# Optimization experiments

Hardware: AMD Instinct MI355X
Metric: run time of the kernel (lower is better)

Reference implementation:

```python
import jax, jax.numpy as jnp
import numpy as np

HEADS = 3
FILT = 16
V_FEATS = 11
N_NODES = 100000
E_INT = 400000
E_NH = 1600000
ATT_SIZE = FILT * 2 * HEADS            # 96
DENSE_IN = ATT_SIZE * HEADS            # 288


def setup_inputs() -> dict:
    key = jax.random.key(0)
    ks = jax.random.split(key, 12)
    node_feats = jax.random.normal(ks[0], (N_NODES, V_FEATS), dtype=jnp.float32)
    edge_int = jax.random.randint(ks[1], (2, E_INT), 0, N_NODES, dtype=jnp.int64)
    edge_nh = jax.random.randint(ks[2], (2, E_NH), 0, N_NODES, dtype=jnp.int64)
    s = 0.1
    W_int = jax.random.normal(ks[3], (V_FEATS, HEADS * FILT), dtype=jnp.float32) * s
    a_src_int = jax.random.normal(ks[4], (HEADS, FILT), dtype=jnp.float32) * s
    a_dst_int = jax.random.normal(ks[5], (HEADS, FILT), dtype=jnp.float32) * s
    W_nh = jax.random.normal(ks[6], (V_FEATS, HEADS * FILT), dtype=jnp.float32) * s
    a_src_nh = jax.random.normal(ks[7], (HEADS, FILT), dtype=jnp.float32) * s
    a_dst_nh = jax.random.normal(ks[8], (HEADS, FILT), dtype=jnp.float32) * s
    att_w = jax.random.normal(ks[9], (ATT_SIZE, HEADS), dtype=jnp.float32) * s
    dense_w = jax.random.normal(ks[10], (DENSE_IN, 1), dtype=jnp.float32) * s
    dense_b = jnp.zeros((1,), dtype=jnp.float32)
    return {
        "node_feats": node_feats,
        "W_int": W_int, "a_src_int": a_src_int, "a_dst_int": a_dst_int,
        "W_nh": W_nh, "a_src_nh": a_src_nh, "a_dst_nh": a_dst_nh,
        "att_w": att_w, "dense_w": dense_w, "dense_b": dense_b,
        "edge_int": edge_int, "edge_nh": edge_nh,
    }


def _gat(x, edges, W, a_src, a_dst):
    """Graph-attention branch: gather -> edge softmax (per dst) -> scatter-add."""
    n = x.shape[0]
    h = (x @ W).reshape(n, HEADS, FILT)              # [N,H,F]
    src, dst = edges[0], edges[1]
    e_s = jnp.einsum('nhf,hf->nh', h, a_src)         # [N,H]
    e_d = jnp.einsum('nhf,hf->nh', h, a_dst)
    e = jax.nn.leaky_relu(e_s[src] + e_d[dst], 0.2)  # [E,H]
    m = jax.ops.segment_max(e, dst, num_segments=n)  # per-dst max for stability
    m = jnp.where(jnp.isfinite(m), m, 0.0)
    p = jnp.exp(e - m[dst])
    denom = jax.ops.segment_sum(p, dst, num_segments=n)
    alpha = p / (denom[dst] + 1e-16)                 # [E,H]
    out = jax.ops.segment_sum(alpha[:, :, None] * h[src], dst, num_segments=n)
    return out.reshape(n, HEADS * FILT)              # [N,48]


def reference(node_feats, W_int, a_src_int, a_dst_int, W_nh, a_src_nh, a_dst_nh,
              att_w, dense_w, dense_b, edge_int, edge_nh):
    x_int = _gat(node_feats, edge_int, W_int, a_src_int, a_dst_int)   # [N,48]
    x_nh = _gat(node_feats, edge_nh, W_nh, a_src_nh, a_dst_nh)        # [N,48]
    x = jnp.concatenate((x_int, x_nh), axis=1)                        # [N,96]
    # multi-head self-attention pooling over nodes
    scores = jnp.tanh(x @ att_w)                                      # [N,3]
    alpha = jax.nn.softmax(scores, axis=0)                            # softmax over nodes
    rep = jnp.einsum('nh,nd->hd', alpha, x).reshape(-1)               # [288]
    out = rep @ dense_w + dense_b                                     # [1]
    return out
```

## Files before the change

kernel.cpp:

```cpp
#include <hip/hip_runtime.h>
#include <math.h>

#define HEADS 3
#define FILT 16
#define HF 48
#define VF 11

#define NBGP 2048
#define NBINMAX 512
#define CAP0 4096
#define CAP1 8192
#define SCCH 8192

typedef unsigned int uint;
typedef unsigned short ushort;

__device__ inline uint f2bf(float x) {
    uint u = __float_as_uint(x);
    return (u + 0x7FFFu + ((u >> 16) & 1u)) >> 16;
}

__device__ inline float tanh_fast(float s) {
    const float sc = fminf(fmaxf(s, -15.f), 15.f);
    const float t = __expf(2.f * sc);
    return (t - 1.f) / (t + 1.f);
}


__global__ __launch_bounds__(256) void k_nodes(
    const float* __restrict__ nf,
    const float* __restrict__ W_int, const float* __restrict__ as_int, const float* __restrict__ ad_int,
    const float* __restrict__ W_nh,  const float* __restrict__ as_nh,  const float* __restrict__ ad_nh,
    float* __restrict__ ws, int* __restrict__ binfill, int N)
{
    __shared__ float sW0[VF*HF], sW1[VF*HF];
    __shared__ float sa[4][HF];
    __shared__ float sF[64*VF];
    __shared__ uint  sH[64*32];
    const int t = threadIdx.x;
    for (int i = t; i < VF*HF; i += 256) { sW0[i] = W_int[i]; sW1[i] = W_nh[i]; }
    if (t < HF) { sa[0][t] = as_int[t]; sa[1][t] = ad_int[t]; sa[2][t] = as_nh[t]; sa[3][t] = ad_nh[t]; }

    const long Nl = N;
    const long B0 = (long)blockIdx.x * 64;
    {
        const long idx = (long)blockIdx.x * 256 + t;
        if (idx < 2*NBINMAX) binfill[idx] = 0;
    }
    for (int i = t; i < 64*VF; i += 256) {
        const long g = B0*VF + i;
        sF[i] = (g < Nl*VF) ? nf[g] : 0.f;
    }
    __syncthreads();

    const int nl = t >> 2;
    const int q  = t & 3;
    const long n = B0 + nl;
    const bool valid = n < Nl;

    float f[VF];
    #pragma unroll
    for (int v = 0; v < VF; v++) f[v] = sF[nl*VF + v];

    for (int b = 0; b < 2; b++) {
        if (b == 1) __syncthreads();
        const float* W = b ? sW1 : sW0;
        float acc[12];
        #pragma unroll
        for (int j = 0; j < 12; j++) acc[j] = 0.f;
        #pragma unroll
        for (int v = 0; v < VF; v++) {
            const float fv = f[v];
            #pragma unroll
            for (int j = 0; j < 12; j++)
                acc[j] = fmaf(fv, W[v*HF + q*12 + j], acc[j]);
        }
        #pragma unroll
        for (int i = 0; i < 6; i++)
            sH[nl*32 + q*6 + i] = f2bf(acc[2*i]) | (f2bf(acc[2*i+1]) << 16);
        sH[nl*32 + 24 + 2*q + 0] = 0u;
        sH[nl*32 + 24 + 2*q + 1] = 0u;

        float s0=0.f,s1=0.f,s2=0.f,d0=0.f,d1=0.f,d2=0.f;
        #pragma unroll
        for (int j = 0; j < 12; j++) {
            const int fg = q*12 + j;
            const int hd = fg >> 4;
            const float ps = acc[j] * sa[2*b + 0][fg];
            const float pd = acc[j] * sa[2*b + 1][fg];
            s0 += (hd == 0) ? ps : 0.f;  d0 += (hd == 0) ? pd : 0.f;
            s1 += (hd == 1) ? ps : 0.f;  d1 += (hd == 1) ? pd : 0.f;
            s2 += (hd == 2) ? ps : 0.f;  d2 += (hd == 2) ? pd : 0.f;
        }
        s0 += __shfl_xor(s0,1); s0 += __shfl_xor(s0,2);
        s1 += __shfl_xor(s1,1); s1 += __shfl_xor(s1,2);
        s2 += __shfl_xor(s2,1); s2 += __shfl_xor(s2,2);
        d0 += __shfl_xor(d0,1); d0 += __shfl_xor(d0,2);
        d1 += __shfl_xor(d1,1); d1 += __shfl_xor(d1,2);
        d2 += __shfl_xor(d2,1); d2 += __shfl_xor(d2,2);
        if (valid && q == 0) {
            float* ES = ws + 64*Nl + (b ? 8*Nl : 0);
            float* ED = ES + 4*Nl;
            ((float4*)ES)[n] = make_float4(s0, s1, s2, 0.f);
            ((float4*)ED)[n] = make_float4(d0, d1, d2, 0.f);
        }
        __syncthreads();
        uint* Hg = (uint*)(ws + (b ? 32*Nl : 0));
        for (int i = t; i < 64*32; i += 256) {
            const long node = B0 + (i >> 5);
            if (node < Nl) Hg[B0*32 + i] = sH[i];
        }
    }
}

__global__ __launch_bounds__(256) void k_binscatter(
    const int* __restrict__ e0, int E0, int nb0,
    const int* __restrict__ e1, int E1,
    int* __restrict__ binfill, uint* __restrict__ pk0, uint* __restrict__ pk1)
{
    __shared__ int lh[NBINMAX], lb[NBINMAX];
    const int b = blockIdx.x;
    const int* e; long E; int* bf; uint* pk; int bb, cap;
    if (b < nb0) { e = e0; E = E0; bf = binfill;           pk = pk0; bb = b;       cap = CAP0; }
    else         { e = e1; E = E1; bf = binfill + NBINMAX; pk = pk1; bb = b - nb0; cap = CAP1; }
    for (int i = threadIdx.x; i < NBINMAX; i += 256) lh[i] = 0;
    __syncthreads();
    const int t = threadIdx.x;
    const long base = (long)bb * SCCH;
    #pragma unroll 4
    for (int k = 0; k < SCCH/256; k++) {
        const long i = base + (long)k*256 + t;
        if (i < E) atomicAdd(&lh[e[E + i] >> 8], 1);
    }
    __syncthreads();
    for (int i = t; i < NBINMAX; i += 256) {
        const int c = lh[i];
        lb[i] = c ? atomicAdd(&bf[i], c) : 0;
        lh[i] = 0;
    }
    __syncthreads();
    #pragma unroll 4
    for (int k = 0; k < SCCH/256; k++) {
        const long i = base + (long)k*256 + t;
        if (i < E) {
            const int s = e[i];
            const int d = e[E + i];
            const int bin = d >> 8;
            const int off = atomicAdd(&lh[bin], 1);
            pk[(long)bin*cap + lb[bin] + off] = ((uint)(d & 255) << 17) | (uint)s;
        }
    }
}

__global__ __launch_bounds__(256) void k_binbucket(
    const uint* __restrict__ pk0, const uint* __restrict__ pk1,
    const int* __restrict__ binfill, int nbin,
    int2* __restrict__ ms0, int* __restrict__ bk0,
    int2* __restrict__ ms1, int* __restrict__ bk1, int N)
{
    __shared__ int nc[256], ns[256], wsum[4];
    const int b = blockIdx.x;
    const int br = (b < nbin) ? 0 : 1;
    const int bin = b - br*nbin;
    const uint* pk = br ? pk1 : pk0;
    const int cap  = br ? CAP1 : CAP0;
    int2* ms = br ? ms1 : ms0;
    int* bk  = br ? bk1 : bk0;
    const long pbase = (long)bin * cap;
    const int m = binfill[br*NBINMAX + bin];
    const int t = threadIdx.x, lane = t & 63, wid = t >> 6;

    nc[t] = 0;
    __syncthreads();
    for (int i = t; i < m; i += 256)
        atomicAdd(&nc[(pk[pbase + i] >> 17) & 255], 1);
    __syncthreads();
    const int v = nc[t];
    int x = v;
    #pragma unroll
    for (int d = 1; d < 64; d <<= 1) { const int u = __shfl_up(x, d); if (lane >= d) x += u; }
    if (lane == 63) wsum[wid] = x;
    __syncthreads();
    int wb = 0;
    #pragma unroll
    for (int w = 0; w < 4; w++) if (w < wid) wb += wsum[w];
    ns[t] = wb + x - v;
    const int n = bin*256 + t;
    if (n < N) ms[n] = make_int2(v, (int)pbase + ns[t] + v);
    nc[t] = 0;
    __syncthreads();
    for (int i = t; i < m; i += 256) {
        const uint p = pk[pbase + i];
        const int dl = (p >> 17) & 255;
        const int off = atomicAdd(&nc[dl], 1);
        bk[pbase + ns[dl] + off] = (int)(p & 0x1FFFFu);
    }
}

__global__ __launch_bounds__(256) void k_gp(
    const uint* __restrict__ H0, const uint* __restrict__ H1,
    const float* __restrict__ ES0, const float4* __restrict__ ED0,
    const float* __restrict__ ES1, const float4* __restrict__ ED1,
    const int2* __restrict__ ms0, const int* __restrict__ bk0,
    const int2* __restrict__ ms1, const int* __restrict__ bk1,
    const float* __restrict__ att_w, const float* __restrict__ dense_w,
    float* __restrict__ gpart, int N)
{
    __shared__ int   sIdx[4][4*64];
    __shared__ float sP[4][4*192];
    const int t = threadIdx.x, lane = t & 63, wid = t >> 6;
    const int half = lane >> 5;
    const int hl = lane & 31;
    const int hcc = (hl >> 3) < 3 ? (hl >> 3) : 2;

    float cL0[3]={0,0,0}, cH0[3]={0,0,0}, cL1[3]={0,0,0}, cH1[3]={0,0,0};
    if (hl < 24) {
        const int f0 = 2*hl, f1 = f0 + 1;
        #pragma unroll
        for (int k = 0; k < 3; k++) {
            if (half == 0) {
                cL0[k] = att_w[f0*3 + k];        cH0[k] = att_w[f1*3 + k];
                cL1[k] = att_w[(HF+f0)*3 + k];   cH1[k] = att_w[(HF+f1)*3 + k];
            } else {
                cL0[k] = dense_w[k*96 + f0];     cH0[k] = dense_w[k*96 + f1];
                cL1[k] = dense_w[k*96 + HF+f0];  cH1[k] = dense_w[k*96 + HF+f1];
            }
        }
    }

    int* iw = sIdx[wid];
    float* pw = sP[wid];

    float acc6[6] = {0,0,0,0,0,0};
    const int gw = blockIdx.x*4 + wid;
    const int nw = NBGP*4;

    for (int n = gw; n < N; n += 2*nw) {
        const int nB = n + nw;
        const bool hasB = nB < N;
        const int2 m0t = ms0[n];
        const int2 m1t = ms1[n];
        const int2 m2t = hasB ? ms0[nB] : make_int2(0, 0);
        const int2 m3t = hasB ? ms1[nB] : make_int2(0, 0);
        int deg[4] = {m0t.x, m1t.x, m2t.x, m3t.x};
        int bas[4] = {m0t.y - m0t.x, m1t.y - m1t.x, m2t.y - m2t.x, m3t.y - m3t.x};
        const int mx = max(max(deg[0], deg[1]), max(deg[2], deg[3]));

        float xL[4], xH[4];

        if (mx <= 64) {
            float4 ev[4];
            ev[0] = ED0[n]; ev[1] = ED1[n];
            ev[2] = hasB ? ED0[nB] : make_float4(0,0,0,0);
            ev[3] = hasB ? ED1[nB] : make_float4(0,0,0,0);
            int sv[4];
            sv[0] = (lane < deg[0]) ? bk0[bas[0] + lane] : 0;
            sv[1] = (lane < deg[1]) ? bk1[bas[1] + lane] : 0;
            sv[2] = (lane < deg[2]) ? bk0[bas[2] + lane] : 0;
            sv[3] = (lane < deg[3]) ? bk1[bas[3] + lane] : 0;
            float4 es[4];
            es[0] = ((const float4*)ES0)[sv[0]];
            es[1] = ((const float4*)ES1)[sv[1]];
            es[2] = ((const float4*)ES0)[sv[2]];
            es[3] = ((const float4*)ES1)[sv[3]];
            #pragma unroll
            for (int T = 0; T < 4; T++) {
                float v0 = es[T].x + ev[T].x, v1 = es[T].y + ev[T].y, v2 = es[T].z + ev[T].z;
                v0 = fmaxf(v0, 0.2f*v0);
                v1 = fmaxf(v1, 0.2f*v1);
                v2 = fmaxf(v2, 0.2f*v2);
                const bool a = lane < deg[T];
                const float p0 = a ? __expf(v0) : 0.f;
                const float p1 = a ? __expf(v1) : 0.f;
                const float p2 = a ? __expf(v2) : 0.f;
                iw[T*64 + lane] = sv[T];
                pw[T*192 + lane*3 + 0] = p0;
                pw[T*192 + lane*3 + 1] = p1;
                pw[T*192 + lane*3 + 2] = p2;
            }
            float accL[4] = {0,0,0,0}, accH[4] = {0,0,0,0}, den[4] = {0,0,0,0};
            const int R = (mx + 7) >> 3;
            for (int r = 0; r < R; r++) {
                const int j0 = r*8;
                uint w[4][4]; float q[4][4];
                #pragma unroll
                for (int T = 0; T < 4; T++) {
                    const uint* H = (T & 1) ? H1 : H0;
                    if (j0 < deg[T]) {
                        #pragma unroll
                        for (int u = 0; u < 4; u++) {
                            const int ei = j0 + 2*u + half;
                            q[T][u] = pw[T*192 + ei*3 + hcc];
                            w[T][u] = H[(long)iw[T*64 + ei]*32 + hl];
                        }
                    }
                }
                #pragma unroll
                for (int T = 0; T < 4; T++) {
                    if (j0 < deg[T]) {
                        #pragma unroll
                        for (int u = 0; u < 4; u++) {
                            accL[T] = fmaf(q[T][u], __uint_as_float(w[T][u] << 16), accL[T]);
                            accH[T] = fmaf(q[T][u], __uint_as_float(w[T][u] & 0xFFFF0000u), accH[T]);
                            den[T] += q[T][u];
                        }
                    }
                }
            }
            #pragma unroll
            for (int T = 0; T < 4; T++) {
                accL[T] += __shfl_xor(accL[T], 32);
                accH[T] += __shfl_xor(accH[T], 32);
                den[T]  += __shfl_xor(den[T], 32);
                const float dinv = 1.f / (den[T] + 1e-16f);
                xL[T] = accL[T] * dinv;
                xH[T] = accH[T] * dinv;
            }
        } else {
            #pragma unroll
            for (int T = 0; T < 4; T++) {
                const uint* H   = (T & 1) ? H1 : H0;
                const float* ES = (T & 1) ? ES1 : ES0;
                const float4* ED = (T & 1) ? ED1 : ED0;
                const int* bk   = (T & 1) ? bk1 : bk0;
                const int nn    = (T >> 1) ? nB : n;
                float accL = 0.f, accH = 0.f, dn = 0.f;
                if (deg[T] > 0) {
                    const float4 edv = ED[nn];
                    for (int e0 = 0; e0 < deg[T]; e0 += 64) {
                        int m = deg[T] - e0; if (m > 64) m = 64;
                        int srcv = 0; float p0 = 0.f, p1 = 0.f, p2 = 0.f;
                        if (lane < m) {
                            srcv = bk[bas[T] + e0 + lane];
                            const float4 esv = ((const float4*)ES)[srcv];
                            float v0 = esv.x + edv.x, v1 = esv.y + edv.y, v2 = esv.z + edv.z;
                            v0 = fmaxf(v0, 0.2f*v0);
                            v1 = fmaxf(v1, 0.2f*v1);
                            v2 = fmaxf(v2, 0.2f*v2);
                            p0 = __expf(v0); p1 = __expf(v1); p2 = __expf(v2);
                        }
                        iw[lane] = srcv;
                        pw[lane*3 + 0] = p0; pw[lane*3 + 1] = p1; pw[lane*3 + 2] = p2;
                        for (int j = 0; j < m; j += 2) {
                            const int ei = j + half;
                            const float qq = pw[ei*3 + hcc];
                            const uint wv = H[(long)iw[ei]*32 + hl];
                            accL = fmaf(qq, __uint_as_float(wv << 16), accL);
                            accH = fmaf(qq, __uint_as_float(wv & 0xFFFF0000u), accH);
                            dn += qq;
                        }
                    }
                }
                accL += __shfl_xor(accL, 32);
                accH += __shfl_xor(accH, 32);
                dn   += __shfl_xor(dn, 32);
                const float dinv = 1.f / (dn + 1e-16f);
                xL[T] = accL * dinv;
                xH[T] = accH * dinv;
            }
        }

        #pragma unroll
        for (int s = 0; s < 2; s++) {
            if (s == 1 && !hasB) break;
            float rr[3];
            #pragma unroll
            for (int k = 0; k < 3; k++)
                rr[k] = xL[2*s]*cL0[k] + xH[2*s]*cH0[k] + xL[2*s+1]*cL1[k] + xH[2*s+1]*cH1[k];
            #pragma unroll
            for (int k = 0; k < 3; k++) {
                #pragma unroll
                for (int o = 1; o < 32; o <<= 1) rr[k] += __shfl_xor(rr[k], o);
            }
            float oo[3];
            #pragma unroll
            for (int k = 0; k < 3; k++) oo[k] = __shfl_xor(rr[k], 32);
            if (lane == 0) {
                #pragma unroll
                for (int k = 0; k < 3; k++) {
                    const float e = __expf(tanh_fast(rr[k]));
                    acc6[k]   += e;
                    acc6[3+k] += e * oo[k];
                }
            }
        }
    }

    __shared__ float red[4][6];
    if (lane == 0) {
        #pragma unroll
        for (int k = 0; k < 6; k++) red[wid][k] = acc6[k];
    }
    __syncthreads();
    if (t < 6) gpart[(long)blockIdx.x*6 + t] = red[0][t] + red[1][t] + red[2][t] + red[3][t];
}

__global__ __launch_bounds__(1024) void k_final(const float* __restrict__ gpart, int nb,
                                                const float* __restrict__ dense_b,
                                                float* __restrict__ out)
{
    const int t = threadIdx.x, lane = t & 63, wid = t >> 6;
    float acc[6] = {0.f,0.f,0.f,0.f,0.f,0.f};
    for (long i = t; i < nb; i += 1024) {
        #pragma unroll
        for (int k = 0; k < 6; k++) acc[k] += gpart[i*6 + k];
    }
    __shared__ float red[16][6];
    #pragma unroll
    for (int k = 0; k < 6; k++) {
        float v = acc[k];
        #pragma unroll
        for (int o = 32; o > 0; o >>= 1) v += __shfl_xor(v, o);
        if (lane == 0) red[wid][k] = v;
    }
    __syncthreads();
    if (t == 0) {
        float tot[6] = {0.f,0.f,0.f,0.f,0.f,0.f};
        #pragma unroll
        for (int w = 0; w < 16; w++)
            #pragma unroll
            for (int k = 0; k < 6; k++) tot[k] += red[w][k];
        float o = dense_b[0];
        #pragma unroll
        for (int h = 0; h < HEADS; h++) o += tot[3 + h] / tot[h];
        out[0] = o;
    }
}

extern "C" void kernel_launch(void* const* d_in, const int* in_sizes, int n_in,
                              void* d_out, int out_size, void* d_ws, size_t ws_size,
                              hipStream_t stream)
{
    const float* nf      = (const float*)d_in[0];
    const float* W_int   = (const float*)d_in[1];
    const float* as_int  = (const float*)d_in[2];
    const float* ad_int  = (const float*)d_in[3];
    const float* W_nh    = (const float*)d_in[4];
    const float* as_nh   = (const float*)d_in[5];
    const float* ad_nh   = (const float*)d_in[6];
    const float* att_w   = (const float*)d_in[7];
    const float* dense_w = (const float*)d_in[8];
    const float* dense_b = (const float*)d_in[9];
    const int*   e_int   = (const int*)d_in[10];
    const int*   e_nh    = (const int*)d_in[11];

    const int N  = in_sizes[0] / VF;
    const int E0 = in_sizes[10] / 2;
    const int E1 = in_sizes[11] / 2;
    const int nbin = (N + 255) >> 8;

    float* ws = (float*)d_ws;
    const long Nl = N;

    uint* h0 = (uint*)ws;
    uint* h1 = (uint*)(ws + 32*Nl);
    float* es0 = ws + 64*Nl;
    float4* ed0 = (float4*)(ws + 68*Nl);
    float* es1 = ws + 72*Nl;
    float4* ed1 = (float4*)(ws + 76*Nl);
    int2* ms0 = (int2*)(ws + 80*Nl);
    int2* ms1 = (int2*)(ws + 82*Nl);
    int* binfill = (int*)(ws + 84*Nl);
    uint* pk0 = (uint*)(binfill + 2*NBINMAX);
    uint* pk1 = pk0 + (long)nbin*CAP0;
    int* bk0  = (int*)(pk1 + (long)nbin*CAP1);
    int* bk1  = bk0 + (long)nbin*CAP0;
    float* gpart = (float*)(bk1 + (long)nbin*CAP1);

    const int nbK1 = (N + 63) / 64;
    const int nbs0 = (E0 + SCCH - 1) / SCCH;
    const int nbs1 = (E1 + SCCH - 1) / SCCH;

    k_nodes<<<nbK1, 256, 0, stream>>>(nf, W_int, as_int, ad_int, W_nh, as_nh, ad_nh,
                                      ws, binfill, N);
    k_binscatter<<<nbs0 + nbs1, 256, 0, stream>>>(e_int, E0, nbs0, e_nh, E1,
                                                  binfill, pk0, pk1);
    k_binbucket<<<2*nbin, 256, 0, stream>>>(pk0, pk1, binfill, nbin,
                                            ms0, bk0, ms1, bk1, N);
    k_gp<<<NBGP, 256, 0, stream>>>(h0, h1, es0, ed0, es1, ed1,
                                   ms0, bk0, ms1, bk1,
                                   att_w, dense_w, gpart, N);
    k_final<<<1, 1024, 0, stream>>>(gpart, NBGP, dense_b, (float*)d_out);
}
```

Before: 146.4 us.

## Process GAT branches in separate passes with per-node partial projections stored

The gather kernel now runs the two graph branches in two sequential passes, handling four nodes of the same branch per wave iteration instead of two nodes across both branches. The first pass writes per-node partial attention scores and dense projections into a scratch buffer that reuses the packed-edge workspace. The second pass adds its own partials and accumulates the pooling sums. The aim is better locality, since each pass gathers from only one feature table, at the cost of an extra per-node write and read and a second sweep over the nodes.

Result: slower. 188.7 us (+28.9%).

```diff
diff --git a/kernel.cpp b/kernel.cpp
--- a/kernel.cpp
+++ b/kernel.cpp
@@ -204,7 +204,7 @@
     const int2* __restrict__ ms0, const int* __restrict__ bk0,
     const int2* __restrict__ ms1, const int* __restrict__ bk1,
     const float* __restrict__ att_w, const float* __restrict__ dense_w,
-    float* __restrict__ gpart, int N)
+    float* __restrict__ pd, float* __restrict__ gpart, int N)
 {
     __shared__ int   sIdx[4][4*64];
     __shared__ float sP[4][4*192];
@@ -235,152 +235,162 @@
     const int gw = blockIdx.x*4 + wid;
     const int nw = NBGP*4;
 
-    for (int n = gw; n < N; n += 2*nw) {
-        const int nB = n + nw;
-        const bool hasB = nB < N;
-        const int2 m0t = ms0[n];
-        const int2 m1t = ms1[n];
-        const int2 m2t = hasB ? ms0[nB] : make_int2(0, 0);
-        const int2 m3t = hasB ? ms1[nB] : make_int2(0, 0);
-        int deg[4] = {m0t.x, m1t.x, m2t.x, m3t.x};
-        int bas[4] = {m0t.y - m0t.x, m1t.y - m1t.x, m2t.y - m2t.x, m3t.y - m3t.x};
-        const int mx = max(max(deg[0], deg[1]), max(deg[2], deg[3]));
-
-        float xL[4], xH[4];
-
-        if (mx <= 64) {
-            float4 ev[4];
-            ev[0] = ED0[n]; ev[1] = ED1[n];
-            ev[2] = hasB ? ED0[nB] : make_float4(0,0,0,0);
-            ev[3] = hasB ? ED1[nB] : make_float4(0,0,0,0);
-            int sv[4];
-            sv[0] = (lane < deg[0]) ? bk0[bas[0] + lane] : 0;
-            sv[1] = (lane < deg[1]) ? bk1[bas[1] + lane] : 0;
-            sv[2] = (lane < deg[2]) ? bk0[bas[2] + lane] : 0;
-            sv[3] = (lane < deg[3]) ? bk1[bas[3] + lane] : 0;
-            float4 es[4];
-            es[0] = ((const float4*)ES0)[sv[0]];
-            es[1] = ((const float4*)ES1)[sv[1]];
-            es[2] = ((const float4*)ES0)[sv[2]];
-            es[3] = ((const float4*)ES1)[sv[3]];
+    for (int b = 0; b < 2; b++) {
+        const uint* H    = b ? H1  : H0;
+        const float* ES  = b ? ES1 : ES0;
+        const float4* ED = b ? ED1 : ED0;
+        const int2* ms   = b ? ms1 : ms0;
+        const int* bk    = b ? bk1 : bk0;
+        const float cbL[3] = { b ? cL1[0] : cL0[0], b ? cL1[1] : cL0[1], b ? cL1[2] : cL0[2] };
+        const float cbH[3] = { b ? cH1[0] : cH0[0], b ? cH1[1] : cH0[1], b ? cH1[2] : cH0[2] };
+
+        for (int n = gw; n < N; n += 4*nw) {
+            int nd[4]; bool val[4];
+            #pragma unroll
+            for (int T = 0; T < 4; T++) { nd[T] = n + T*nw; val[T] = nd[T] < N; }
+            int deg[4], bas[4];
             #pragma unroll
             for (int T = 0; T < 4; T++) {
-                float v0 = es[T].x + ev[T].x, v1 = es[T].y + ev[T].y, v2 = es[T].z + ev[T].z;
-                v0 = fmaxf(v0, 0.2f*v0);
-                v1 = fmaxf(v1, 0.2f*v1);
-                v2 = fmaxf(v2, 0.2f*v2);
-                const bool a = lane < deg[T];
-                const float p0 = a ? __expf(v0) : 0.f;
-                const float p1 = a ? __expf(v1) : 0.f;
-                const float p2 = a ? __expf(v2) : 0.f;
-                iw[T*64 + lane] = sv[T];
-                pw[T*192 + lane*3 + 0] = p0;
-                pw[T*192 + lane*3 + 1] = p1;
-                pw[T*192 + lane*3 + 2] = p2;
+                const int2 m2 = val[T] ? ms[nd[T]] : make_int2(0, 0);
+                deg[T] = m2.x; bas[T] = m2.y - m2.x;
             }
-            float accL[4] = {0,0,0,0}, accH[4] = {0,0,0,0}, den[4] = {0,0,0,0};
-            const int R = (mx + 7) >> 3;
-            for (int r = 0; r < R; r++) {
-                const int j0 = r*8;
-                uint w[4][4]; float q[4][4];
+            const int mx = max(max(deg[0], deg[1]), max(deg[2], deg[3]));
+
+            float xL[4], xH[4];
+
+            if (mx <= 64) {
+                float4 ev[4];
+                #pragma unroll
+                for (int T = 0; T < 4; T++) ev[T] = val[T] ? ED[nd[T]] : make_float4(0,0,0,0);
+                int sv[4];
+                #pragma unroll
+                for (int T = 0; T < 4; T++) sv[T] = (lane < deg[T]) ? bk[bas[T] + lane] : 0;
+                float4 es[4];
+                #pragma unroll
+                for (int T = 0; T < 4; T++) es[T] = ((const float4*)ES)[sv[T]];
                 #pragma unroll
                 for (int T = 0; T < 4; T++) {
-                    const uint* H = (T & 1) ? H1 : H0;
-                    if (j0 < deg[T]) {
-                        #pragma unroll
-                        for (int u = 0; u < 4; u++) {
-                            const int ei = j0 + 2*u + half;
-                            q[T][u] = pw[T*192 + ei*3 + hcc];
-                            w[T][u] = H[(long)iw[T*64 + ei]*32 + hl];
+                    float v0 = es[T].x + ev[T].x, v1 = es[T].y + ev[T].y, v2 = es[T].z + ev[T].z;
+                    v0 = fmaxf(v0, 0.2f*v0);
+                    v1 = fmaxf(v1, 0.2f*v1);
+                    v2 = fmaxf(v2, 0.2f*v2);
+                    const bool a = lane < deg[T];
+                    const float p0 = a ? __expf(v0) : 0.f;
+                    const float p1 = a ? __expf(v1) : 0.f;
+                    const float p2 = a ? __expf(v2) : 0.f;
+                    iw[T*64 + lane] = sv[T];
+                    pw[T*192 + lane*3 + 0] = p0;
+                    pw[T*192 + lane*3 + 1] = p1;
+                    pw[T*192 + lane*3 + 2] = p2;
+                }
+                float accL[4] = {0,0,0,0}, accH[4] = {0,0,0,0}, den[4] = {0,0,0,0};
+                const int R = (mx + 7) >> 3;
+                for (int r = 0; r < R; r++) {
+                    const int j0 = r*8;
+                    uint w[4][4]; float q[4][4];
+                    #pragma unroll
+                    for (int T = 0; T < 4; T++) {
+                        if (j0 < deg[T]) {
+                            #pragma unroll
+                            for (int u = 0; u < 4; u++) {
+                                const int ei = j0 + 2*u + half;
+                                q[T][u] = pw[T*192 + ei*3 + hcc];
+                                w[T][u] = H[(long)iw[T*64 + ei]*32 + hl];
+                            }
                         }
                     }
-                }
-                #pragma unroll
-                for (int T = 0; T < 4; T++) {
-                    if (j0 < deg[T]) {
-                        #pragma unroll
-                        for (int u = 0; u < 4; u++) {
-                            accL[T] = fmaf(q[T][u], __uint_as_float(w[T][u] << 16), accL[T]);
-                            accH[T] = fmaf(q[T][u], __uint_as_float(w[T][u] & 0xFFFF0000u), accH[T]);
-                            den[T] += q[T][u];
+                    #pragma unroll
+                    for (int T = 0; T < 4; T++) {
+                        if (j0 < deg[T]) {
+                            #pragma unroll
+                            for (int u = 0; u < 4; u++) {
+                                accL[T] = fmaf(q[T][u], __uint_as_float(w[T][u] << 16), accL[T]);
+                                accH[T] = fmaf(q[T][u], __uint_as_float(w[T][u] & 0xFFFF0000u), accH[T]);
+                                den[T] += q[T][u];
+                            }
                         }
                     }
                 }
+                #pragma unroll
+                for (int T = 0; T < 4; T++) {
+                    accL[T] += __shfl_xor(accL[T], 32);
+                    accH[T] += __shfl_xor(accH[T], 32);
+                    den[T]  += __shfl_xor(den[T], 32);
+                    const float dinv = 1.f / (den[T] + 1e-16f);
+                    xL[T] = accL[T] * dinv;
+                    xH[T] = accH[T] * dinv;
+                }
+            } else {
+                #pragma unroll
+                for (int T = 0; T < 4; T++) {
+                    float accL = 0.f, accH = 0.f, dn = 0.f;
+                    if (deg[T] > 0) {
+                        const float4 edv = ED[nd[T]];
+                        for (int e0 = 0; e0 < deg[T]; e0 += 64) {
+                            int m = deg[T] - e0; if (m > 64) m = 64;
+                            int srcv = 0; float p0 = 0.f, p1 = 0.f, p2 = 0.f;
+                            if (lane < m) {
+                                srcv = bk[bas[T] + e0 + lane];
+                                const float4 esv = ((const float4*)ES)[srcv];
+                                float v0 = esv.x + edv.x, v1 = esv.y + edv.y, v2 = esv.z + edv.z;
+                                v0 = fmaxf(v0, 0.2f*v0);
+                                v1 = fmaxf(v1, 0.2f*v1);
+                                v2 = fmaxf(v2, 0.2f*v2);
+                                p0 = __expf(v0); p1 = __expf(v1); p2 = __expf(v2);
+                            }
+                            iw[lane] = srcv;
+                            pw[lane*3 + 0] = p0; pw[lane*3 + 1] = p1; pw[lane*3 + 2] = p2;
+                            for (int j = 0; j < m; j += 2) {
+                                const int ei = j + half;
+                                const float qq = pw[ei*3 + hcc];
+                                const uint wv = H[(long)iw[ei]*32 + hl];
+                                accL = fmaf(qq, __uint_as_float(wv << 16), accL);
+                                accH = fmaf(qq, __uint_as_float(wv & 0xFFFF0000u), accH);
+                                dn += qq;
+                            }
+                        }
+                    }
+                    accL += __shfl_xor(accL, 32);
+                    accH += __shfl_xor(accH, 32);
+                    dn   += __shfl_xor(dn, 32);
+                    const float dinv = 1.f / (dn + 1e-16f);
+                    xL[T] = accL * dinv;
+                    xH[T] = accH * dinv;
+                }
             }
+
             #pragma unroll
             for (int T = 0; T < 4; T++) {
-                accL[T] += __shfl_xor(accL[T], 32);
-                accH[T] += __shfl_xor(accH[T], 32);
-                den[T]  += __shfl_xor(den[T], 32);
-                const float dinv = 1.f / (den[T] + 1e-16f);
-                xL[T] = accL[T] * dinv;
-                xH[T] = accH[T] * dinv;
-            }
-        } else {
-            #pragma unroll
-            for (int T = 0; T < 4; T++) {
-                const uint* H   = (T & 1) ? H1 : H0;
-                const float* ES = (T & 1) ? ES1 : ES0;
-                const float4* ED = (T & 1) ? ED1 : ED0;
-                const int* bk   = (T & 1) ? bk1 : bk0;
-                const int nn    = (T >> 1) ? nB : n;
-                float accL = 0.f, accH = 0.f, dn = 0.f;
-                if (deg[T] > 0) {
-                    const float4 edv = ED[nn];
-                    for (int e0 = 0; e0 < deg[T]; e0 += 64) {
-                        int m = deg[T] - e0; if (m > 64) m = 64;
-                        int srcv = 0; float p0 = 0.f, p1 = 0.f, p2 = 0.f;
-                        if (lane < m) {
-                            srcv = bk[bas[T] + e0 + lane];
-                            const float4 esv = ((const float4*)ES)[srcv];
-                            float v0 = esv.x + edv.x, v1 = esv.y + edv.y, v2 = esv.z + edv.z;
-                            v0 = fmaxf(v0, 0.2f*v0);
-                            v1 = fmaxf(v1, 0.2f*v1);
-                            v2 = fmaxf(v2, 0.2f*v2);
-                            p0 = __expf(v0); p1 = __expf(v1); p2 = __expf(v2);
-                        }
-                        iw[lane] = srcv;
-                        pw[lane*3 + 0] = p0; pw[lane*3 + 1] = p1; pw[lane*3 + 2] = p2;
-                        for (int j = 0; j < m; j += 2) {
-                            const int ei = j + half;
-                            const float qq = pw[ei*3 + hcc];
-                            const uint wv = H[(long)iw[ei]*32 + hl];
-                            accL = fmaf(qq, __uint_as_float(wv << 16), accL);
-                            accH = fmaf(qq, __uint_as_float(wv & 0xFFFF0000u), accH);
-                            dn += qq;
+                if (!val[T]) continue;
+                float rr[3];
+                #pragma unroll
+                for (int k = 0; k < 3; k++)
+                    rr[k] = xL[T]*cbL[k] + xH[T]*cbH[k];
+                #pragma unroll
+                for (int k = 0; k < 3; k++) {
+                    #pragma unroll
+                    for (int o = 1; o < 32; o <<= 1) rr[k] += __shfl_xor(rr[k], o);
+                }
+                if (b == 0) {
+                    if (hl == 0) {
+                        const long n6 = (long)nd[T]*6 + (half ? 3 : 0);
+                        pd[n6 + 0] = rr[0]; pd[n6 + 1] = rr[1]; pd[n6 + 2] = rr[2];
+                    }
+                } else {
+                    float oo[3];
+                    #pragma unroll
+                    for (int k = 0; k < 3; k++) oo[k] = __shfl_xor(rr[k], 32);
+                    if (lane == 0) {
+                        const long n6 = (long)nd[T]*6;
+                        #pragma unroll
+                        for (int k = 0; k < 3; k++) {
+                            const float s = pd[n6 + k] + rr[k];
+                            const float y = pd[n6 + 3 + k] + oo[k];
+                            const float e = __expf(tanh_fast(s));
+                            acc6[k]   += e;
+                            acc6[3+k] += e * y;
                         }
                     }
-                }
-                accL += __shfl_xor(accL, 32);
-                accH += __shfl_xor(accH, 32);
-                dn   += __shfl_xor(dn, 32);
-                const float dinv = 1.f / (dn + 1e-16f);
-                xL[T] = accL * dinv;
-                xH[T] = accH * dinv;
-            }
-        }
-
-        #pragma unroll
-        for (int s = 0; s < 2; s++) {
-            if (s == 1 && !hasB) break;
-            float rr[3];
-            #pragma unroll
-            for (int k = 0; k < 3; k++)
-                rr[k] = xL[2*s]*cL0[k] + xH[2*s]*cH0[k] + xL[2*s+1]*cL1[k] + xH[2*s+1]*cH1[k];
-            #pragma unroll
-            for (int k = 0; k < 3; k++) {
-                #pragma unroll
-                for (int o = 1; o < 32; o <<= 1) rr[k] += __shfl_xor(rr[k], o);
-            }
-            float oo[3];
-            #pragma unroll
-            for (int k = 0; k < 3; k++) oo[k] = __shfl_xor(rr[k], 32);
-            if (lane == 0) {
-                #pragma unroll
-                for (int k = 0; k < 3; k++) {
-                    const float e = __expf(tanh_fast(rr[k]));
-                    acc6[k]   += e;
-                    acc6[3+k] += e * oo[k];
                 }
             }
         }
@@ -466,6 +476,7 @@
     int* bk0  = (int*)(pk1 + (long)nbin*CAP1);
     int* bk1  = bk0 + (long)nbin*CAP0;
     float* gpart = (float*)(bk1 + (long)nbin*CAP1);
+    float* pd    = (float*)pk0;
 
     const int nbK1 = (N + 63) / 64;
     const int nbs0 = (E0 + SCCH - 1) / SCCH;
@@ -479,6 +490,6 @@
                                             ms0, bk0, ms1, bk1, N);
     k_gp<<<NBGP, 256, 0, stream>>>(h0, h1, es0, ed0, es1, ed1,
                                    ms0, bk0, ms1, bk1,
-                                   att_w, dense_w, gpart, N);
+                                   att_w, dense_w, pd, gpart, N);
     k_final<<<1, 1024, 0, stream>>>(gpart, NBGP, dense_b, (float*)d_out);
 }
```
